# Optimization experiments

Measured on AMD Instinct MI355X. Metric: run time of the kernel, lower is better.

## Reference

```python
import jax, jax.numpy as jnp
import numpy as np
from jax import lax

WIN = 7            # skimage default win_size
K1, K2 = 0.01, 0.03
DATA_RANGE = 1.0


def _uniform_filter_valid(x):
    # (skimage uses reflect-padded uniform_filter then crops pad=3, which equals
    #  a valid windowed mean.)
    c, h, w = x.shape
    x4 = x[:, None]                                   # (C,1,H,W)
    kh = jnp.full((1, 1, WIN, 1), 1.0 / WIN, x.dtype)
    kw = jnp.full((1, 1, 1, WIN), 1.0 / WIN, x.dtype)
    dn = ('NCHW', 'OIHW', 'NCHW')
    x4 = lax.conv_general_dilated(x4, kh, (1, 1), 'VALID', dimension_numbers=dn)
    x4 = lax.conv_general_dilated(x4, kw, (1, 1), 'VALID', dimension_numbers=dn)
    return x4[:, 0]


def setup_inputs() -> dict:
    key = jax.random.key(0)
    k1, k2 = jax.random.split(key)
    shape = (32, 3, 512, 512)
    return {
        'input_tensor': jax.random.uniform(k1, shape, dtype=jnp.float32),
        'target': jax.random.uniform(k2, shape, dtype=jnp.float32),
    }


def reference(input_tensor, target):
    h, w = input_tensor.shape[-2:]
    x = input_tensor.reshape(-1, h, w).astype(jnp.float32)
    y = target.reshape(-1, h, w).astype(jnp.float32)

    C1 = (K1 * DATA_RANGE) ** 2
    C2 = (K2 * DATA_RANGE) ** 2
    NP = WIN * WIN
    cov_norm = NP / (NP - 1.0)  # sample covariance (skimage default)

    ux = _uniform_filter_valid(x)
    uy = _uniform_filter_valid(y)
    uxx = _uniform_filter_valid(x * x)
    uyy = _uniform_filter_valid(y * y)
    uxy = _uniform_filter_valid(x * y)

    vx = cov_norm * (uxx - ux * ux)
    vy = cov_norm * (uyy - uy * uy)
    vxy = cov_norm * (uxy - ux * uy)

    S = ((2.0 * ux * uy + C1) * (2.0 * vxy + C2)) / (
        (ux * ux + uy * uy + C1) * (vx + vy + C2))
    # mean over cropped spatial map per channel, then over channels == global mean
    return jnp.mean(S)
```

## Files before the change

### kernel.cpp

```cpp
#include <hip/hip_runtime.h>


namespace {
constexpr int W       = 512;
constexpr int HH      = 512;
constexpr int NIMG    = 96;
constexpr int OW      = 506;
constexpr int RSTRIP  = 23;
constexpr int NSTRIP  = 22;
constexpr int WAVES   = NIMG * NSTRIP;
constexpr int BLOCKS  = WAVES / 4;
constexpr float C1f   = 1.0e-4f;
constexpr float C2f   = 9.0e-4f;
constexpr float COVN  = 49.0f / 48.0f;
constexpr float INV49 = 1.0f / 49.0f;
constexpr double NPIX = 96.0 * 506.0 * 506.0;
}

__device__ __forceinline__ void load8(const float* __restrict__ p, float v[8])
{
    float4 a = *(const float4*)(p);
    float4 b = *(const float4*)(p + 4);
    v[0] = a.x; v[1] = a.y; v[2] = a.z; v[3] = a.w;
    v[4] = b.x; v[5] = b.y; v[6] = b.z; v[7] = b.w;
}

__global__ __launch_bounds__(256, 2) void ssim_main(const float* __restrict__ X,
                                                    const float* __restrict__ Y,
                                                    double* __restrict__ partial)
{
    __shared__ float wsum[4];

    const int t     = threadIdx.x;
    const int lane  = t & 63;
    const int wid   = t >> 6;
    const int gw    = blockIdx.x * 4 + wid;
    const int img   = gw / NSTRIP;
    const int strip = gw - img * NSTRIP;
    const int r0    = strip * RSTRIP;
    const int c0    = lane * 8;

    const float* xb = X + (size_t)img * (W * HH) + c0;
    const float* yb = Y + (size_t)img * (W * HH) + c0;

    float V[5][8];
#pragma unroll
    for (int q = 0; q < 5; q++)
#pragma unroll
        for (int k = 0; k < 8; k++) V[q][k] = 0.0f;

#pragma unroll
    for (int r = 0; r < 6; r++) {
        float xs[8], ys[8];
        load8(xb + (size_t)(r0 + r) * W, xs);
        load8(yb + (size_t)(r0 + r) * W, ys);
#pragma unroll
        for (int k = 0; k < 8; k++) {
            V[0][k] += xs[k];
            V[1][k] += ys[k];
            V[2][k] = fmaf(xs[k], xs[k], V[2][k]);
            V[3][k] = fmaf(ys[k], ys[k], V[3][k]);
            V[4][k] = fmaf(xs[k], ys[k], V[4][k]);
        }
    }

    float xn[8], yn[8];
    load8(xb + (size_t)(r0 + 6) * W, xn);
    load8(yb + (size_t)(r0 + 6) * W, yn);

    float sacc = 0.0f;

#pragma unroll 1
    for (int j = 0; j < RSTRIP; j++) {
#pragma unroll
        for (int k = 0; k < 8; k++) {
            V[0][k] += xn[k];
            V[1][k] += yn[k];
            V[2][k] = fmaf(xn[k], xn[k], V[2][k]);
            V[3][k] = fmaf(yn[k], yn[k], V[3][k]);
            V[4][k] = fmaf(xn[k], yn[k], V[4][k]);
        }

        float xo[8], yo[8], x2[8], y2[8];
        load8(xb + (size_t)(r0 + j) * W, xo);
        load8(yb + (size_t)(r0 + j) * W, yo);
        int rn = r0 + j + 7; if (rn > HH - 1) rn = HH - 1;
        load8(xb + (size_t)rn * W, x2);
        load8(yb + (size_t)rn * W, y2);

        float Hh[5][8];
#pragma unroll
        for (int q = 0; q < 5; q++) {
            float P[8];
            P[0] = V[q][0];
#pragma unroll
            for (int k = 1; k < 8; k++) P[k] = P[k - 1] + V[q][k];
            const float Pn0 = __shfl_down(P[0], 1);
            const float Pn1 = __shfl_down(P[1], 1);
            const float Pn2 = __shfl_down(P[2], 1);
            const float Pn3 = __shfl_down(P[3], 1);
            const float Pn4 = __shfl_down(P[4], 1);
            const float Pn5 = __shfl_down(P[5], 1);
            const float T = P[7];
            Hh[q][0] = P[6];
            Hh[q][1] = T - P[0];
            Hh[q][2] = (T - P[1]) + Pn0;
            Hh[q][3] = (T - P[2]) + Pn1;
            Hh[q][4] = (T - P[3]) + Pn2;
            Hh[q][5] = (T - P[4]) + Pn3;
            Hh[q][6] = (T - P[5]) + Pn4;
            Hh[q][7] = (T - P[6]) + Pn5;
        }

#pragma unroll
        for (int k = 0; k < 8; k++) {
            float ux  = Hh[0][k] * INV49;
            float uy  = Hh[1][k] * INV49;
            float uxx = Hh[2][k] * INV49;
            float uyy = Hh[3][k] * INV49;
            float uxy = Hh[4][k] * INV49;
            float uxuy = ux * uy;
            float a1 = fmaf(2.0f, uxuy, C1f);
            float b1 = fmaf(ux, ux, fmaf(uy, uy, C1f));
            float vxy = COVN * (uxy - uxuy);
            float a2 = fmaf(2.0f, vxy, C2f);
            float vs  = COVN * ((uxx - ux * ux) + (uyy - uy * uy));
            float b2 = vs + C2f;
            float S = (a1 * a2) / (b1 * b2);
            if (c0 + k < OW) sacc += S;
        }

#pragma unroll
        for (int k = 0; k < 8; k++) {
            V[0][k] -= xo[k];
            V[1][k] -= yo[k];
            V[2][k] = fmaf(-xo[k], xo[k], V[2][k]);
            V[3][k] = fmaf(-yo[k], yo[k], V[3][k]);
            V[4][k] = fmaf(-xo[k], yo[k], V[4][k]);
        }
#pragma unroll
        for (int k = 0; k < 8; k++) { xn[k] = x2[k]; yn[k] = y2[k]; }
    }

#pragma unroll
    for (int off = 32; off > 0; off >>= 1)
        sacc += __shfl_down(sacc, off);
    if (lane == 0) wsum[wid] = sacc;
    __syncthreads();
    if (t == 0)
        partial[blockIdx.x] = (double)((wsum[0] + wsum[1]) + (wsum[2] + wsum[3]));
}

__global__ void ssim_finalize(const double* __restrict__ partial, float* __restrict__ out)
{
    __shared__ double ws[4];
    const int t = threadIdx.x;
    double s = 0.0;
    for (int i = t; i < BLOCKS; i += 256) s += partial[i];
#pragma unroll
    for (int off = 32; off > 0; off >>= 1)
        s += __shfl_down(s, off);
    if ((t & 63) == 0) ws[t >> 6] = s;
    __syncthreads();
    if (t == 0) out[0] = (float)(((ws[0] + ws[1]) + (ws[2] + ws[3])) / NPIX);
}

extern "C" void kernel_launch(void* const* d_in, const int* in_sizes, int n_in,
                              void* d_out, int out_size, void* d_ws, size_t ws_size,
                              hipStream_t stream)
{
    const float* X = (const float*)d_in[0];
    const float* Y = (const float*)d_in[1];
    float* out = (float*)d_out;
    double* partial = (double*)d_ws;

    ssim_main<<<dim3(BLOCKS), 256, 0, stream>>>(X, Y, partial);
    ssim_finalize<<<1, 256, 0, stream>>>(partial, out);
}
```

Baseline: 255.8 us.

## Halve row strips, fold 1/49 scaling into constants, use fast reciprocal

Shrinks each wave's row strip from 23 to 11 rows, doubling the number of waves so more of the GPU is occupied. The per-pixel SSIM math is rescaled by 49^2 so the five 1/49 multiplies disappear, with the constants scaled to match. The full-precision divide is replaced by a hardware rcp approximation plus one Newton refinement. More strips mean more redundant 6-row warm-up loads per strip, and the rcp path changes rounding slightly.

```diff
diff --git a/kernel.cpp b/kernel.cpp
--- a/kernel.cpp
+++ b/kernel.cpp
@@ -6,14 +6,13 @@
 constexpr int HH      = 512;
 constexpr int NIMG    = 96;
 constexpr int OW      = 506;
-constexpr int RSTRIP  = 23;
-constexpr int NSTRIP  = 22;
+constexpr int RSTRIP  = 11;
+constexpr int NSTRIP  = 46;
 constexpr int WAVES   = NIMG * NSTRIP;
 constexpr int BLOCKS  = WAVES / 4;
-constexpr float C1f   = 1.0e-4f;
-constexpr float C2f   = 9.0e-4f;
+constexpr float C1s   = 0.2401f;
+constexpr float C2s   = 2.1609f;
 constexpr float COVN  = 49.0f / 48.0f;
-constexpr float INV49 = 1.0f / 49.0f;
 constexpr double NPIX = 96.0 * 506.0 * 506.0;
 }
 
@@ -114,19 +113,22 @@
 
 #pragma unroll
         for (int k = 0; k < 8; k++) {
-            float ux  = Hh[0][k] * INV49;
-            float uy  = Hh[1][k] * INV49;
-            float uxx = Hh[2][k] * INV49;
-            float uyy = Hh[3][k] * INV49;
-            float uxy = Hh[4][k] * INV49;
-            float uxuy = ux * uy;
-            float a1 = fmaf(2.0f, uxuy, C1f);
-            float b1 = fmaf(ux, ux, fmaf(uy, uy, C1f));
-            float vxy = COVN * (uxy - uxuy);
-            float a2 = fmaf(2.0f, vxy, C2f);
-            float vs  = COVN * ((uxx - ux * ux) + (uyy - uy * uy));
-            float b2 = vs + C2f;
-            float S = (a1 * a2) / (b1 * b2);
+            float A = Hh[0][k], B = Hh[1][k];
+            float Pq = Hh[2][k], Qq = Hh[3][k], R = Hh[4][k];
+            float AB   = A * B;
+            float a1   = fmaf(2.0f, AB, C1s);
+            float ab2  = fmaf(A, A, B * B);
+            float b1   = ab2 + C1s;
+            float tt   = fmaf(49.0f, R, -AB);
+            float a2   = fmaf(2.0f * COVN, tt, C2s);
+            float pq   = Pq + Qq;
+            float t2   = fmaf(49.0f, pq, -ab2);
+            float b2   = fmaf(COVN, t2, C2s);
+            float num  = a1 * a2;
+            float den  = b1 * b2;
+            float r    = __builtin_amdgcn_rcpf(den);
+            r = r * fmaf(-den, r, 2.0f);
+            float S = num * r;
             if (c0 + k < OW) sacc += S;
         }
 
```

After: 253.0 us. About the same (-1.1%).
